# Kernel tuning notes

Measured on AMD Instinct MI355X. Metric: run time of the kernel, lower is better.

The kernel has to match this reference:

```python
import math
import jax, jax.numpy as jnp
import numpy as np

B, S, D = 8, 512, 1024        # batch, seq (dec and enc), model dim
HID, NH = 1024, 16            # attention hidden, heads
C = HID // NH                 # per-head channels (self-attn 'attends' over this dim!)
EPS = 1e-5


def setup_inputs() -> dict:
    key = jax.random.key(0)
    ks = jax.random.split(key, 26)
    w = lambda k, sh: (jax.random.normal(k, sh, jnp.float32) * 0.02)
    inp = {
        "x": jax.random.normal(ks[0], (B, S, D), jnp.float32),
        "h": jax.random.normal(ks[1], (B, S, D), jnp.float32),
        # self-attn (AttentionModule) params, stored [in, out]
        "Wq": w(ks[2], (D, HID)), "bq": jnp.zeros((HID,), jnp.float32),
        "Wk": w(ks[3], (D, HID)), "bk": jnp.zeros((HID,), jnp.float32),
        "Wv": w(ks[4], (D, HID)), "bv": jnp.zeros((HID,), jnp.float32),
        "Wo": w(ks[5], (HID, D)), "bo": jnp.zeros((D,), jnp.float32),
        # cross-attn params
        "Wcq": w(ks[6], (D, HID)), "bcq": jnp.zeros((HID,), jnp.float32),
        "Wck": w(ks[7], (D, HID)), "bck": jnp.zeros((HID,), jnp.float32),
        "Wcv": w(ks[8], (D, HID)), "bcv": jnp.zeros((HID,), jnp.float32),
        "Wco": w(ks[9], (HID, D)), "bco": jnp.zeros((D,), jnp.float32),
        "gamma": jnp.ones((D,), jnp.float32), "beta": jnp.zeros((D,), jnp.float32),
        # FFN (two Linears, NO nonlinearity, per original code)
        "W1": w(ks[10], (D, HID)), "b1": jnp.zeros((HID,), jnp.float32),
        "W2": w(ks[11], (HID, D)), "b2": jnp.zeros((D,), jnp.float32),
    }
    return inp


def _layernorm(x, gamma, beta):
    mu = jnp.mean(x, axis=-1, keepdims=True)
    var = jnp.mean(jnp.square(x - mu), axis=-1, keepdims=True)
    return (x - mu) * jax.lax.rsqrt(var + EPS) * gamma + beta


def _self_attn(x, Wq, bq, Wk, bk, Wv, bv, Wo, bo):
    # FAITHFUL to original: reshape [B,S,NH,C]; einsum '...hq,...hk->...hqk' with
    # batch dims [B,S] -> attention over the C channel dim per token, causal mask over channels.
    Q = (x @ Wq + bq).reshape(B, S, NH, C) / math.sqrt(C)
    K = (x @ Wk + bk).reshape(B, S, NH, C)
    V = (x @ Wv + bv).reshape(B, S, NH, C)
    aff = jnp.einsum('bshq,bshk->bshqk', Q, K)            # [B,S,NH,C,C]
    mask = jnp.triu(jnp.full((C, C), -jnp.inf, jnp.float32), k=1)  # -inf above diag, 0 else
    aff = aff + mask
    w = jax.nn.softmax(aff, axis=-1)
    av = jnp.einsum('bshqk,bshk->bshq', w, V)             # [B,S,NH,C]
    return av.reshape(B, S, HID) @ Wo + bo


def _cross_attn(xd, he, Wcq, bcq, Wck, bck, Wcv, bcv, Wco, bco):
    # standard multi-head cross attention, but scaled by sqrt(d_full) per original
    Q = (xd @ Wcq + bcq).reshape(B, S, NH, C).transpose(0, 2, 1, 3)  # [B,NH,Sq,C]
    K = (he @ Wck + bck).reshape(B, S, NH, C).transpose(0, 2, 1, 3)
    V = (he @ Wcv + bcv).reshape(B, S, NH, C).transpose(0, 2, 1, 3)
    scores = jnp.einsum('bhqd,bhkd->bhqk', Q, K) / math.sqrt(HID)
    p = jax.nn.softmax(scores, axis=-1)
    o = jnp.einsum('bhqk,bhkd->bhqd', p, V)               # [B,NH,Sq,C]
    o = o.transpose(0, 2, 1, 3).reshape(B, S, HID)
    return o @ Wco + bco


def reference(x, h, Wq, bq, Wk, bk, Wv, bv, Wo, bo,
              Wcq, bcq, Wck, bck, Wcv, bcv, Wco, bco,
              gamma, beta, W1, b1, W2, b2):
    out = _self_attn(x, Wq, bq, Wk, bk, Wv, bv, Wo, bo) + x
    out = _layernorm(out, gamma, beta)
    out = _cross_attn(out, h, Wcq, bcq, Wck, bck, Wcv, bcv, Wco, bco) + out
    out = _layernorm(out, gamma, beta)
    out = ((out @ W1 + b1) @ W2 + b2) + out
    out = _layernorm(out, gamma, beta)
    return out
```

## Files before the change

kernel.cpp:

```cpp
#include <hip/hip_runtime.h>

typedef __bf16 bf16_t;
typedef bf16_t bf16x8 __attribute__((ext_vector_type(8)));
typedef bf16_t bf16x4 __attribute__((ext_vector_type(4)));
typedef float f32x4 __attribute__((ext_vector_type(4)));
typedef unsigned u32x4 __attribute__((ext_vector_type(4)));

__device__ __forceinline__ void async_copy16(const void* g, void* l) {
  __builtin_amdgcn_global_load_lds(
      (const __attribute__((address_space(1))) unsigned int*)(unsigned long long)g,
      (__attribute__((address_space(3))) unsigned int*)(unsigned int)(unsigned long long)l,
      16, 0, 0);
}

__device__ __forceinline__ float fast_exp2(float x) {
#if __has_builtin(__builtin_amdgcn_exp2f)
  return __builtin_amdgcn_exp2f(x);
#else
  float r;
  asm volatile("v_exp_f32 %0, %1\n\ts_nop 0" : "=v"(r) : "v"(x));
  return r;
#endif
}
__device__ __forceinline__ float fast_rcp(float x) {
#if __has_builtin(__builtin_amdgcn_rcpf)
  return __builtin_amdgcn_rcpf(x);
#else
  float r;
  asm volatile("v_rcp_f32 %0, %1\n\ts_nop 0" : "=v"(r) : "v"(x));
  return r;
#endif
}

__device__ __forceinline__ unsigned pack_bf16(float x, float y) {
  bf16_t lo = (bf16_t)x, hi = (bf16_t)y;
  unsigned short ul, uh;
  __builtin_memcpy(&ul, &lo, 2);
  __builtin_memcpy(&uh, &hi, 2);
  return (unsigned)ul | ((unsigned)uh << 16);
}

#define QSCALE 0.180336688f

struct SrcPtrs { const float* p[10]; };
__global__ __launch_bounds__(256) void prep_main(
    SrcPtrs srcs, bf16_t* __restrict__ dstbase,
    const float* __restrict__ a, const float* __restrict__ b,
    const float* __restrict__ w1, bf16_t* __restrict__ dst1,
    bf16_t* __restrict__ dstw) {
  __shared__ float tile[32][33];
  int bid = blockIdx.x;
  int tid = threadIdx.x;
  if (bid < 10240) {
    int z = bid >> 10;
    int rem = bid & 1023;
    const float* src = srcs.p[z];
    bf16_t* dst = dstbase + (size_t)z * 1048576;
    float scale = (z == 0) ? QSCALE : ((z == 4) ? 0.03125f : 1.f);
    int bx = (rem & 31) * 32;
    int by = (rem >> 5) * 32;
    int tx = tid & 31, ty = tid >> 5;
#pragma unroll
    for (int i = 0; i < 32; i += 8)
      tile[ty + i][tx] = src[(size_t)(by + ty + i) * 1024 + bx + tx];
    __syncthreads();
#pragma unroll
    for (int i = 0; i < 32; i += 8)
      dst[(size_t)(bx + ty + i) * 1024 + by + tx] = (bf16_t)(tile[tx][ty + i] * scale);
  } else {
    int i = ((bid - 10240) * 256 + tid) * 8;
    const float* s;
    bf16_t* d;
    if (i < 4194304) { s = a + i; d = dst1 + i; }
    else if (i < 8388608) { s = b + i - 4194304; d = dst1 + i; }
    else { s = w1 + i - 8388608; d = dstw + (i - 8388608); }
    float4 u = *(const float4*)s;
    float4 v = *(const float4*)(s + 4);
    bf16x8 o;
    o[0]=(bf16_t)u.x; o[1]=(bf16_t)u.y; o[2]=(bf16_t)u.z; o[3]=(bf16_t)u.w;
    o[4]=(bf16_t)v.x; o[5]=(bf16_t)v.y; o[6]=(bf16_t)v.z; o[7]=(bf16_t)v.w;
    *(bf16x8*)d = o;
  }
}

__global__ __launch_bounds__(256) void prep_bias_kernel(
    const float* __restrict__ bq, const float* __restrict__ bk,
    const float* __restrict__ bv, const float* __restrict__ bck,
    const float* __restrict__ bcv, const float* __restrict__ bcq,
    const bf16_t* __restrict__ wt9, const float* __restrict__ b1,
    const float* __restrict__ b2, float* __restrict__ cb,
    float* __restrict__ cb2) {
  int bid = blockIdx.x;
  if (bid < 28) {
    int i = bid * 256 + threadIdx.x;
    if (i < 1024) cb[i] = bq[i] * QSCALE;
    else if (i < 2048) cb[i] = bk[i - 1024];
    else if (i < 3072) cb[i] = bv[i - 2048];
    else if (i < 4096) cb[i] = bck[i - 3072];
    else if (i < 5120) cb[i] = bcv[i - 4096];
    else if (i < 6144) cb[i] = bcq[i - 5120] * 0.03125f;
    else cb[i] = 0.f;
  } else {
    int n = (bid - 28) * 256 + threadIdx.x;
    const bf16_t* row = wt9 + (size_t)n * 1024;
    float acc = 0.f;
#pragma unroll 4
    for (int h = 0; h < 1024; h += 8) {
      bf16x8 v = *(const bf16x8*)(row + h);
      float4 ba = *(const float4*)(b1 + h);
      float4 bb = *(const float4*)(b1 + h + 4);
      acc += ba.x*(float)v[0] + ba.y*(float)v[1] + ba.z*(float)v[2] + ba.w*(float)v[3]
           + bb.x*(float)v[4] + bb.y*(float)v[5] + bb.z*(float)v[6] + bb.w*(float)v[7];
    }
    cb2[n] = acc + b2[n];
  }
}

template <int BM, int BN, int MI, int NI, bool HAS_RES, bool TRANS_OUT, bool DBUF>
__device__ __forceinline__ void gemm_core(
    const bf16_t* __restrict__ A, const bf16_t* __restrict__ Bt,
    const float* __restrict__ bias, const bf16_t* __restrict__ res,
    bf16_t* __restrict__ C, int ldC, int bm, int bn,
    bf16_t* As, bf16_t* Bs) {
  constexpr int ASZ = BM * 64, BSZ = BN * 64;
  int tid = threadIdx.x;
  int w = tid >> 6, lane = tid & 63;
  int fm = lane & 15, fq = lane >> 4;
  int wm, wn;
  if (BM == 128 && BN == 128) { wm = (w >> 1) * 64; wn = (w & 1) * 64; }
  else if (BM == 128) { wm = w * 32; wn = 0; }
  else { wm = (w >> 1) * 32; wn = (w & 1) * (BN / 2); }
  f32x4 acc[MI][NI] = {};

  auto stage = [&](int kt, int half) {
    bf16_t* Ad = DBUF ? As + half * ASZ : As;
    bf16_t* Bd = DBUF ? Bs + half * BSZ : Bs;
#pragma unroll
    for (int i = 0; i < BM / 32; i++) {
      int c = i * 256 + tid;
      int row = c >> 3, skg = (c & 7) ^ (row & 7);
      async_copy16(A + (size_t)(bm + row) * 1024 + kt + skg * 8, &Ad[c * 8]);
    }
#pragma unroll
    for (int i = 0; i < BN / 32; i++) {
      int c = i * 256 + tid;
      int row = c >> 3, skg = (c & 7) ^ (row & 7);
      async_copy16(Bt + (size_t)(bn + row) * 1024 + kt + skg * 8, &Bd[c * 8]);
    }
  };
  auto compute = [&](int half) {
    const bf16_t* Ac = DBUF ? As + half * ASZ : As;
    const bf16_t* Bc = DBUF ? Bs + half * BSZ : Bs;
#pragma unroll
    for (int ks = 0; ks < 2; ks++) {
      bf16x8 af[MI], bfr[NI];
      int kg = ks * 4 + fq;
#pragma unroll
      for (int mi = 0; mi < MI; mi++) {
        int row = wm + mi * 16 + fm;
        af[mi] = *(const bf16x8*)&Ac[row * 64 + ((kg ^ (row & 7)) * 8)];
      }
#pragma unroll
      for (int ni = 0; ni < NI; ni++) {
        int row = wn + ni * 16 + fm;
        bfr[ni] = *(const bf16x8*)&Bc[row * 64 + ((kg ^ (row & 7)) * 8)];
      }
#pragma unroll
      for (int mi = 0; mi < MI; mi++)
#pragma unroll
        for (int ni = 0; ni < NI; ni++)
          acc[mi][ni] = __builtin_amdgcn_mfma_f32_16x16x32_bf16(
              af[mi], bfr[ni], acc[mi][ni], 0, 0, 0);
    }
  };

  if (DBUF) {
    stage(0, 0);
    __syncthreads();
#pragma unroll
    for (int t = 0; t < 16; t++) {
      if (t < 15) stage((t + 1) * 64, (t + 1) & 1);
      compute(t & 1);
      __syncthreads();
    }
  } else {
    for (int kt = 0; kt < 1024; kt += 64) {
      stage(kt, 0);
      __syncthreads();
      compute(0);
      __syncthreads();
    }
  }

#pragma unroll
  for (int mi = 0; mi < MI; mi++) {
#pragma unroll
    for (int ni = 0; ni < NI; ni++) {
      int col = bn + wn + ni * 16 + fm;
      float bv = bias[col];
      if (TRANS_OUT) {
        int rowb = bm + wm + mi * 16 + fq * 4;
        bf16x4 w4;
#pragma unroll
        for (int r = 0; r < 4; r++) w4[r] = (bf16_t)(acc[mi][ni][r] + bv);
        *(bf16x4*)&C[(size_t)col * ldC + rowb] = w4;
      } else {
#pragma unroll
        for (int r = 0; r < 4; r++) {
          int row = bm + wm + mi * 16 + fq * 4 + r;
          float v = acc[mi][ni][r] + bv;
          if (HAS_RES) v += (float)res[(size_t)row * ldC + col];
          C[(size_t)row * ldC + col] = (bf16_t)v;
        }
      }
    }
  }
}

template <bool HAS_RES, bool TRANS_OUT>
__global__ __launch_bounds__(256) void gemm_bf16(
    const bf16_t* __restrict__ A, const bf16_t* __restrict__ Bt,
    const float* __restrict__ bias, const bf16_t* __restrict__ res,
    bf16_t* __restrict__ C, int ldC) {
  __shared__ bf16_t As[2 * 64 * 64];
  __shared__ bf16_t Bs[2 * 64 * 64];
  int lin = blockIdx.x;
  int xcd = lin & 7, idx = lin >> 3;
  int ly = idx >> 4, lx = idx & 15;
  int bm = (xcd * 8 + ly) * 64;
  int bn = lx * 64;
  gemm_core<64, 64, 2, 2, HAS_RES, TRANS_OUT, true>(A, Bt, bias, res, C, ldC,
                                                    bm, bn, As, Bs);
}

__global__ __launch_bounds__(256) void gemm_mega(
    const bf16_t* __restrict__ xb, const bf16_t* __restrict__ wt0,
    const bf16_t* __restrict__ wt9, const bf16_t* __restrict__ w1bf,
    const bf16_t* __restrict__ hb, const bf16_t* __restrict__ wt4,
    const float* __restrict__ cb, bf16_t* __restrict__ qkv,
    bf16_t* __restrict__ pt, bf16_t* __restrict__ kbuf,
    bf16_t* __restrict__ vt) {
  __shared__ bf16_t As[64 * 64];
  __shared__ bf16_t Bs[128 * 64];
  int bid = blockIdx.x;
  if (bid < 1536) {
    int xcd = bid & 7, idx = bid >> 3;
    int ly = idx / 12, lx = idx - ly * 12;
    int bm = ((xcd >> 1) * 16 + ly) * 64;
    int bn = ((xcd & 1) * 12 + lx) * 128;
    gemm_core<64, 128, 2, 4, false, false, false>(xb, wt0, cb, nullptr, qkv,
                                                  3072, bm, bn, As, Bs);
  } else if (bid < 1664) {
    int idx = bid - 1536;
    gemm_core<64, 128, 2, 4, false, false, false>(wt9, w1bf, cb + 6144, nullptr,
                                                  pt, 1024, (idx & 15) * 64,
                                                  (idx >> 4) * 128, As, Bs);
  } else if (bid < 2176) {
    int idx = bid - 1664;
    int xcd = idx & 7, j = idx >> 3;
    int bm = (xcd * 8 + (j >> 3)) * 64;
    int bn = (j & 7) * 128;
    gemm_core<64, 128, 2, 4, false, false, false>(hb, wt4 + 1048576, cb + 3072,
                                                  nullptr, kbuf, 1024, bm, bn,
                                                  As, Bs);
  } else {
    int idx = bid - 2176;
    int xcd = idx & 7, j = idx >> 3;
    int bm = (xcd * 8 + (j >> 3)) * 64;
    int bn = (j & 7) * 128;
    gemm_core<64, 128, 2, 4, false, true, false>(hb, wt4 + 2097152, cb + 4096,
                                                 nullptr, vt, 4096, bm, bn,
                                                 As, Bs);
  }
}

__global__ __launch_bounds__(256) void self_attn_kernel(
    const bf16_t* __restrict__ QKV, bf16_t* __restrict__ O) {
  int tid = threadIdx.x;
  int lane = tid & 63;
  int unit = __builtin_amdgcn_readfirstlane(blockIdx.x * 4 + (tid >> 6));
  int m = unit >> 4, h = unit & 15;
  size_t base = (size_t)m * 3072 + h * 64;
  size_t iq = base + lane;
  float qv = (float)QKV[iq];
  float kown = (float)QKV[iq + 1024];
  float vown = (float)QKV[iq + 2048];
  const u32x4* Krow = (const u32x4*)(QKV + base + 1024);
  const u32x4* Vrow = (const u32x4*)(QKV + base + 2048);
  u32x4 K4[8], V4[8];
#pragma unroll
  for (int i = 0; i < 8; i++) { K4[i] = Krow[i]; V4[i] = Vrow[i]; }
  float l0 = 0.f, l1 = 0.f, o0 = 0.f, o1 = 0.f;
#pragma unroll
  for (int p = 0; p < 32; p++) {
    unsigned kw = K4[p >> 2][p & 3];
    unsigned vw = V4[p >> 2][p & 3];
    float k0 = __uint_as_float(kw << 16);
    float k1 = __uint_as_float(kw & 0xffff0000u);
    float v0 = __uint_as_float(vw << 16);
    float v1 = __uint_as_float(vw & 0xffff0000u);
    float e0 = fast_exp2(qv * k0);
    float e1 = fast_exp2(qv * k1);
    bool c = lane >= 2 * p + 1;
    e0 = c ? e0 : 0.f;
    e1 = c ? e1 : 0.f;
    l0 += e0; o0 = fmaf(e0, v0, o0);
    l1 += e1; o1 = fmaf(e1, v1, o1);
  }
  float ed = fast_exp2(qv * kown);
  ed = ((lane & 1) == 0) ? ed : 0.f;
  float l = (l0 + l1) + ed;
  float o = fmaf(ed, vown, o0 + o1);
  O[(size_t)m * 1024 + h * 64 + lane] = (bf16_t)(o * fast_rcp(l));
}

__global__ __launch_bounds__(256) void cross_attn_mfma(
    const bf16_t* __restrict__ Q, const bf16_t* __restrict__ Kb,
    const bf16_t* __restrict__ Vt, bf16_t* __restrict__ O) {
  __shared__ bf16_t Ks[64 * 64];
  __shared__ bf16_t Vs[64 * 64];
  int tid = threadIdx.x;
  int w = tid >> 6, lane = tid & 63;
  int fm = lane & 15, fq = lane >> 4;
  int bh = blockIdx.x;
  int b = bh >> 4, h = bh & 15;
  int q0 = blockIdx.y * 64 + w * 16;
  const bf16_t* Qp = Q + (size_t)(b * 512 + q0 + fm) * 1024 + h * 64 + fq * 8;
  bf16x8 qf0 = *(const bf16x8*)Qp;
  bf16x8 qf1 = *(const bf16x8*)(Qp + 32);
  f32x4 o[4] = {};
  float mx = -1e30f, l = 0.f;
  for (int k0 = 0; k0 < 512; k0 += 64) {
    __syncthreads();
#pragma unroll
    for (int i = 0; i < 2; i++) {
      int c = i * 256 + tid;
      int row = c >> 3, kg = (c & 7) ^ (row & 7);
      async_copy16(Kb + (size_t)(b * 512 + k0 + row) * 1024 + h * 64 + kg * 8,
                   &Ks[c * 8]);
      async_copy16(Vt + (size_t)(h * 64 + row) * 4096 + b * 512 + k0 + kg * 8,
                   &Vs[c * 8]);
    }
    __syncthreads();
    f32x4 s[4] = {};
#pragma unroll
    for (int mt = 0; mt < 4; mt++) {
      int row = mt * 16 + fm;
#pragma unroll
      for (int f = 0; f < 2; f++) {
        int kg = f * 4 + fq;
        bf16x8 kf = *(const bf16x8*)&Ks[row * 64 + ((kg ^ (row & 7)) * 8)];
        s[mt] = __builtin_amdgcn_mfma_f32_16x16x32_bf16(
            kf, (f ? qf1 : qf0), s[mt], 0, 0, 0);
      }
    }
    float smax = -1e30f;
#pragma unroll
    for (int mt = 0; mt < 4; mt++)
#pragma unroll
      for (int r = 0; r < 4; r++) smax = fmaxf(smax, s[mt][r]);
    smax = fmaxf(smax, __shfl_xor(smax, 16, 64));
    smax = fmaxf(smax, __shfl_xor(smax, 32, 64));
    float nm = fmaxf(mx, smax);
    float corr = __expf(mx - nm);
    float ladd = 0.f;
    unsigned pk0[4], pk1[4];
#pragma unroll
    for (int mt = 0; mt < 4; mt++) {
      float p0 = __expf(s[mt][0] - nm);
      float p1 = __expf(s[mt][1] - nm);
      float p2 = __expf(s[mt][2] - nm);
      float p3 = __expf(s[mt][3] - nm);
      ladd += (p0 + p1) + (p2 + p3);
      pk0[mt] = pack_bf16(p0, p1);
      pk1[mt] = pack_bf16(p2, p3);
    }
    ladd += __shfl_xor(ladd, 16, 64);
    ladd += __shfl_xor(ladd, 32, 64);
    l = l * corr + ladd;
#pragma unroll
    for (int ct = 0; ct < 4; ct++)
#pragma unroll
      for (int r = 0; r < 4; r++) o[ct][r] *= corr;
    union U { unsigned u[4]; bf16x8 v; } pf[2];
    int sl0 = ((fq & 1) * 2) * 16 + fm;
    int sl1 = sl0 + 16;
    bool hi = fq >= 2;
#pragma unroll
    for (int f = 0; f < 2; f++) {
      unsigned a0 = (unsigned)__shfl((int)pk0[f * 2],     sl0, 64);
      unsigned b0 = (unsigned)__shfl((int)pk0[f * 2 + 1], sl0, 64);
      unsigned a1 = (unsigned)__shfl((int)pk1[f * 2],     sl0, 64);
      unsigned b1 = (unsigned)__shfl((int)pk1[f * 2 + 1], sl0, 64);
      unsigned a2 = (unsigned)__shfl((int)pk0[f * 2],     sl1, 64);
      unsigned b2 = (unsigned)__shfl((int)pk0[f * 2 + 1], sl1, 64);
      unsigned a3 = (unsigned)__shfl((int)pk1[f * 2],     sl1, 64);
      unsigned b3 = (unsigned)__shfl((int)pk1[f * 2 + 1], sl1, 64);
      pf[f].u[0] = hi ? b0 : a0;
      pf[f].u[1] = hi ? b1 : a1;
      pf[f].u[2] = hi ? b2 : a2;
      pf[f].u[3] = hi ? b3 : a3;
    }
#pragma unroll
    for (int ct = 0; ct < 4; ct++) {
      int row = ct * 16 + fm;
#pragma unroll
      for (int f = 0; f < 2; f++) {
        int kg = f * 4 + fq;
        bf16x8 vf = *(const bf16x8*)&Vs[row * 64 + ((kg ^ (row & 7)) * 8)];
        o[ct] = __builtin_amdgcn_mfma_f32_16x16x32_bf16(vf, pf[f].v, o[ct], 0, 0, 0);
      }
    }
    mx = nm;
  }
  float inv = 1.f / l;
  bf16_t* Op = O + (size_t)(b * 512 + q0 + fm) * 1024 + h * 64 + fq * 4;
#pragma unroll
  for (int ct = 0; ct < 4; ct++) {
    bf16x4 w4;
    w4[0] = (bf16_t)(o[ct][0] * inv);
    w4[1] = (bf16_t)(o[ct][1] * inv);
    w4[2] = (bf16_t)(o[ct][2] * inv);
    w4[3] = (bf16_t)(o[ct][3] * inv);
    *(bf16x4*)(Op + ct * 16) = w4;
  }
}

template <typename OutT>
__global__ __launch_bounds__(256) void ln_kernel(
    const bf16_t* __restrict__ X, const float* __restrict__ gamma,
    const float* __restrict__ beta, OutT* __restrict__ Y) {
  __shared__ float red[8];
  int row = blockIdx.x;
  int tid = threadIdx.x;
  bf16x4 x4 = *(const bf16x4*)(X + (size_t)row * 1024 + tid * 4);
  float4 v = {(float)x4[0], (float)x4[1], (float)x4[2], (float)x4[3]};
  float s = (v.x + v.y) + (v.z + v.w);
  float ss = fmaf(v.x, v.x, fmaf(v.y, v.y, fmaf(v.z, v.z, v.w * v.w)));
#pragma unroll
  for (int off = 32; off > 0; off >>= 1) {
    s  += __shfl_down(s, off, 64);
    ss += __shfl_down(ss, off, 64);
  }
  if ((tid & 63) == 0) { red[tid >> 6] = s; red[4 + (tid >> 6)] = ss; }
  __syncthreads();
  float S  = (red[0] + red[1]) + (red[2] + red[3]);
  float SS = (red[4] + red[5]) + (red[6] + red[7]);
  float mu = S * (1.f / 1024.f);
  float var = SS * (1.f / 1024.f) - mu * mu;
  float inv = rsqrtf(var + 1e-5f);
  float4 g = *(const float4*)(gamma + tid * 4);
  float4 b = *(const float4*)(beta + tid * 4);
  float r0 = (v.x - mu) * inv * g.x + b.x;
  float r1 = (v.y - mu) * inv * g.y + b.y;
  float r2 = (v.z - mu) * inv * g.z + b.z;
  float r3 = (v.w - mu) * inv * g.w + b.w;
  OutT* yp = Y + (size_t)row * 1024 + tid * 4;
  yp[0] = (OutT)r0; yp[1] = (OutT)r1; yp[2] = (OutT)r2; yp[3] = (OutT)r3;
}

extern "C" void kernel_launch(void* const* d_in, const int* in_sizes, int n_in,
                              void* d_out, int out_size, void* d_ws, size_t ws_size,
                              hipStream_t stream) {
  (void)in_sizes; (void)n_in; (void)out_size; (void)ws_size;
  const float* x  = (const float*)d_in[0];
  const float* hh = (const float*)d_in[1];
  SrcPtrs sp;
  sp.p[0] = (const float*)d_in[2];  sp.p[1] = (const float*)d_in[4];
  sp.p[2] = (const float*)d_in[6];  sp.p[3] = (const float*)d_in[8];
  sp.p[4] = (const float*)d_in[10]; sp.p[5] = (const float*)d_in[12];
  sp.p[6] = (const float*)d_in[14]; sp.p[7] = (const float*)d_in[16];
  sp.p[8] = (const float*)d_in[20]; sp.p[9] = (const float*)d_in[22];
  const float* W1f = (const float*)d_in[20];
  const float* bq  = (const float*)d_in[3];
  const float* bk  = (const float*)d_in[5];
  const float* bv  = (const float*)d_in[7];
  const float* bo  = (const float*)d_in[9];
  const float* bck = (const float*)d_in[13];
  const float* bcv = (const float*)d_in[15];
  const float* bcq = (const float*)d_in[11];
  const float* bco = (const float*)d_in[17];
  const float* gamma = (const float*)d_in[18];
  const float* beta  = (const float*)d_in[19];
  const float* b1  = (const float*)d_in[21];
  const float* b2  = (const float*)d_in[23];
  float* out = (float*)d_out;
  char* ws = (char*)d_ws;
  const size_t MB = 1048576;

  bf16_t* wt[10];
  for (int i = 0; i < 10; i++) wt[i] = (bf16_t*)(ws + (size_t)i * 2 * MB);
  float* cb      = (float*)(ws + 20 * MB);
  float* cb2     = (float*)(ws + 20 * MB + 32768);
  bf16_t* xb     = (bf16_t*)(ws + 21 * MB);
  bf16_t* hb     = (bf16_t*)(ws + 29 * MB);
  bf16_t* qkv    = (bf16_t*)(ws + 37 * MB);
  bf16_t* cqbuf  = (bf16_t*)(ws + 37 * MB);
  bf16_t* g4     = (bf16_t*)(ws + 45 * MB);
  bf16_t* kbuf   = (bf16_t*)(ws + 61 * MB);
  bf16_t* vtbuf  = (bf16_t*)(ws + 69 * MB);
  bf16_t* attn   = (bf16_t*)(ws + 77 * MB);
  bf16_t* ptbuf  = (bf16_t*)(ws + 85 * MB);
  bf16_t* w1bf   = (bf16_t*)(ws + 87 * MB);
  bf16_t* t1n    = xb;
  bf16_t* t2n    = hb;
  bf16_t* f2out  = g4;

  prep_main<<<14848, 256, 0, stream>>>(sp, (bf16_t*)ws, x, hh, W1f, xb, w1bf);
  prep_bias_kernel<<<32, 256, 0, stream>>>(bq, bk, bv, bck, bcv, bcq,
                                           wt[9], b1, b2, cb, cb2);

  gemm_mega<<<2688, 256, 0, stream>>>(xb, wt[0], wt[9], w1bf, hb, wt[4], cb,
                                      qkv, ptbuf, kbuf, vtbuf);
  self_attn_kernel<<<16384, 256, 0, stream>>>(qkv, attn);
  gemm_bf16<true, false><<<1024, 256, 0, stream>>>(attn, wt[3], bo, xb, g4, 1024);
  ln_kernel<bf16_t><<<4096, 256, 0, stream>>>(g4, gamma, beta, t1n);
  gemm_bf16<false, false><<<1024, 256, 0, stream>>>(t1n, wt[4], cb + 5120,
                                                    nullptr, cqbuf, 1024);
  cross_attn_mfma<<<dim3(128, 8), 256, 0, stream>>>(cqbuf, kbuf, vtbuf, attn);
  gemm_bf16<true, false><<<1024, 256, 0, stream>>>(attn, wt[7], bco, t1n, g4, 1024);
  ln_kernel<bf16_t><<<4096, 256, 0, stream>>>(g4, gamma, beta, t2n);
  gemm_bf16<true, false><<<1024, 256, 0, stream>>>(t2n, ptbuf, cb2, t2n, f2out, 1024);
  ln_kernel<float><<<4096, 256, 0, stream>>>(f2out, gamma, beta, out);
}
```

Measured before the change: 367.1 us.

## Double-buffer mega GEMM and pipeline loads with partial vmcnt waits

Switches the gemm_mega kernel's four GEMM variants to the double-buffered path, which doubles their LDS allocation. It also replaces __syncthreads in the DBUF loop with explicit s_waitcnt vmcnt(N) plus raw s_barrier, so the next tile's async global-to-LDS loads can stay in flight while the current tile is computed. This is meant to hide global memory latency behind the MFMA work. The cost is higher LDS use per block, which may lower occupancy, and correctness now depends on the hand-counted vmcnt values.

```diff
diff --git a/kernel.cpp b/kernel.cpp
--- a/kernel.cpp
+++ b/kernel.cpp
@@ -11,6 +11,16 @@
       (const __attribute__((address_space(1))) unsigned int*)(unsigned long long)g,
       (__attribute__((address_space(3))) unsigned int*)(unsigned int)(unsigned long long)l,
       16, 0, 0);
+}
+
+template <int N> __device__ __forceinline__ void vm_wait() {
+  if constexpr (N == 0) asm volatile("s_waitcnt vmcnt(0)" ::: "memory");
+  else if constexpr (N == 4) asm volatile("s_waitcnt vmcnt(4)" ::: "memory");
+  else if constexpr (N == 6) asm volatile("s_waitcnt vmcnt(6)" ::: "memory");
+  else if constexpr (N == 8) asm volatile("s_waitcnt vmcnt(8)" ::: "memory");
+}
+__device__ __forceinline__ void raw_barrier() {
+  asm volatile("s_barrier" ::: "memory");
 }
 
 __device__ __forceinline__ float fast_exp2(float x) {
@@ -123,6 +133,7 @@
     bf16_t* __restrict__ C, int ldC, int bm, int bn,
     bf16_t* As, bf16_t* Bs) {
   constexpr int ASZ = BM * 64, BSZ = BN * 64;
+  constexpr int LPS = BM / 32 + BN / 32;
   int tid = threadIdx.x;
   int w = tid >> 6, lane = tid & 63;
   int fm = lane & 15, fq = lane >> 4;
@@ -176,12 +187,18 @@
 
   if (DBUF) {
     stage(0, 0);
-    __syncthreads();
 #pragma unroll
     for (int t = 0; t < 16; t++) {
-      if (t < 15) stage((t + 1) * 64, (t + 1) & 1);
+      if (t < 15) {
+        stage((t + 1) * 64, (t + 1) & 1);
+        vm_wait<LPS>();
+      } else {
+        vm_wait<0>();
+      }
+      raw_barrier();
       compute(t & 1);
-      __syncthreads();
+      asm volatile("s_waitcnt lgkmcnt(0)" ::: "memory");
+      raw_barrier();
     }
   } else {
     for (int kt = 0; kt < 1024; kt += 64) {
@@ -240,37 +257,37 @@
     const float* __restrict__ cb, bf16_t* __restrict__ qkv,
     bf16_t* __restrict__ pt, bf16_t* __restrict__ kbuf,
     bf16_t* __restrict__ vt) {
-  __shared__ bf16_t As[64 * 64];
-  __shared__ bf16_t Bs[128 * 64];
+  __shared__ bf16_t As[2 * 64 * 64];
+  __shared__ bf16_t Bs[2 * 128 * 64];
   int bid = blockIdx.x;
   if (bid < 1536) {
     int xcd = bid & 7, idx = bid >> 3;
     int ly = idx / 12, lx = idx - ly * 12;
     int bm = ((xcd >> 1) * 16 + ly) * 64;
     int bn = ((xcd & 1) * 12 + lx) * 128;
-    gemm_core<64, 128, 2, 4, false, false, false>(xb, wt0, cb, nullptr, qkv,
-                                                  3072, bm, bn, As, Bs);
+    gemm_core<64, 128, 2, 4, false, false, true>(xb, wt0, cb, nullptr, qkv,
+                                                 3072, bm, bn, As, Bs);
   } else if (bid < 1664) {
     int idx = bid - 1536;
-    gemm_core<64, 128, 2, 4, false, false, false>(wt9, w1bf, cb + 6144, nullptr,
-                                                  pt, 1024, (idx & 15) * 64,
-                                                  (idx >> 4) * 128, As, Bs);
+    gemm_core<64, 128, 2, 4, false, false, true>(wt9, w1bf, cb + 6144, nullptr,
+                                                 pt, 1024, (idx & 15) * 64,
+                                                 (idx >> 4) * 128, As, Bs);
   } else if (bid < 2176) {
     int idx = bid - 1664;
     int xcd = idx & 7, j = idx >> 3;
     int bm = (xcd * 8 + (j >> 3)) * 64;
     int bn = (j & 7) * 128;
-    gemm_core<64, 128, 2, 4, false, false, false>(hb, wt4 + 1048576, cb + 3072,
-                                                  nullptr, kbuf, 1024, bm, bn,
-                                                  As, Bs);
+    gemm_core<64, 128, 2, 4, false, false, true>(hb, wt4 + 1048576, cb + 3072,
+                                                 nullptr, kbuf, 1024, bm, bn,
+                                                 As, Bs);
   } else {
     int idx = bid - 2176;
     int xcd = idx & 7, j = idx >> 3;
     int bm = (xcd * 8 + (j >> 3)) * 64;
     int bn = (j & 7) * 128;
-    gemm_core<64, 128, 2, 4, false, true, false>(hb, wt4 + 2097152, cb + 4096,
-                                                 nullptr, vt, 4096, bm, bn,
-                                                 As, Bs);
+    gemm_core<64, 128, 2, 4, false, true, true>(hb, wt4 + 2097152, cb + 4096,
+                                                nullptr, vt, 4096, bm, bn,
+                                                As, Bs);
   }
 }
 
```

After: 366.7 us. No clear change (-0.1%).
